# Performance work log

Hardware: AMD Instinct MI355X
Metric: run time of the kernel (lower is better)

## Reference

```python
import jax, jax.numpy as jnp
import numpy as np

B, S, D, H = 2, 2048, 1024, 16
HD = D // H

def setup_inputs() -> dict:
    key = jax.random.key(0)
    ks = jax.random.split(key, 5)
    sc = 1.0 / np.sqrt(D)
    return {
        "x": jax.random.normal(ks[0], (B, S, D), dtype=jnp.float32),
        "Wq": jax.random.normal(ks[1], (D, D), dtype=jnp.float32) * sc,
        "bq": jnp.zeros((D,), jnp.float32),
        "Wk": jax.random.normal(ks[2], (D, D), dtype=jnp.float32) * sc,
        "bk": jnp.zeros((D,), jnp.float32),
        "Wv": jax.random.normal(ks[3], (D, D), dtype=jnp.float32) * sc,
        "bv": jnp.zeros((D,), jnp.float32),
        "Wo": jax.random.normal(ks[4], (D, D), dtype=jnp.float32) * sc,
        "bo": jnp.zeros((D,), jnp.float32),
    }

def reference(x, Wq, bq, Wk, bk, Wv, bv, Wo, bo):
    b, s, d = x.shape
    def proj(W, bias):
        # [B,S,D] -> [B,H,S,HD]
        return (x @ W + bias).reshape(b, s, H, HD).swapaxes(1, 2)
    q = proj(Wq, bq)
    k = proj(Wk, bk)
    v = proj(Wv, bv)
    # naive full attention, matching the module (materializes [B,H,S,S])
    logits = jnp.einsum("bhqd,bhkd->bhqk", q, k) / jnp.sqrt(jnp.float32(HD))
    attn = jax.nn.softmax(logits, axis=-1)
    vals = jnp.einsum("bhqk,bhkd->bhqd", attn, v)
    vals = vals.swapaxes(1, 2).reshape(b, s, d)
    return vals @ Wo + bo
```

## Files before the change

### kernel.cpp

```cpp
#include <hip/hip_runtime.h>

typedef unsigned short u16;
typedef __bf16 bf16x8 __attribute__((ext_vector_type(8)));
typedef float f32x4 __attribute__((ext_vector_type(4)));

__device__ __forceinline__ u16 f2bf(float f) {
    union { float f; unsigned int i; } v;
    v.f = f;
    unsigned int u = v.i;
    return (u16)((u + 0x7fffu + ((u >> 16) & 1u)) >> 16);
}

__device__ __forceinline__ void dma16(const void* g, void* l) {
    __builtin_amdgcn_global_load_lds(
        (__attribute__((address_space(1))) void*)g,
        (__attribute__((address_space(3))) void*)l, 16, 0, 0);
}


__global__ __launch_bounds__(256) void cvt_w(const float* __restrict__ in,
                                             u16* __restrict__ out) {
    __shared__ u16 t[32][33];
    int bx = blockIdx.x * 32, by = blockIdx.y * 32;
    int tx = threadIdx.x & 31, ty = threadIdx.x >> 5;
#pragma unroll
    for (int i = 0; i < 32; i += 8)
        t[ty + i][tx] = f2bf(in[(size_t)(by + ty + i) * 1024 + bx + tx]);
    __syncthreads();
#pragma unroll
    for (int i = 0; i < 32; i += 8) {
        int n = bx + ty + i, k = by + tx;
        out[(size_t)n * 1024 + (k ^ ((n & 7) << 3))] = t[tx][ty + i];
    }
}

__global__ __launch_bounds__(256) void cvt_x(const float* __restrict__ in,
                                             u16* __restrict__ out) {
    int i = blockIdx.x * 256 + threadIdx.x;
    int s = i >> 8, k = (i & 255) * 4;
    float4 f = reinterpret_cast<const float4*>(in)[i];
    ushort4 h;
    h.x = f2bf(f.x); h.y = f2bf(f.y); h.z = f2bf(f.z); h.w = f2bf(f.w);
    *reinterpret_cast<ushort4*>(&out[(size_t)s * 1024 + (k ^ ((s & 7) << 3))]) = h;
}

__global__ __launch_bounds__(256) void gemm_qkv(
    const u16* __restrict__ xbf, const u16* __restrict__ wt,
    const float* __restrict__ bq, const float* __restrict__ bk,
    const float* __restrict__ bv,
    u16* __restrict__ qkg, u16* __restrict__ vgt) {
    __shared__ __align__(16) u16 As[128 * 64];
    __shared__ __align__(16) u16 Bs[128 * 64];

    int tid = threadIdx.x;
    int m0 = blockIdx.y * 128, n0 = blockIdx.x * 128;
    int wave = tid >> 6, lane = tid & 63;
    int wm = (wave >> 1) * 64, wn = (wave & 1) * 64;
    int l16 = lane & 15, quad = lane >> 4;
    int sl = l16 & 7;

    int seg = n0 >> 10;
    int n0r = n0 & 1023;
    const u16* WT = wt + (size_t)seg * 1048576;
    bool swp = (seg == 2);

    f32x4 acc[4][4];
#pragma unroll
    for (int mi = 0; mi < 4; mi++)
#pragma unroll
        for (int ni = 0; ni < 4; ni++) acc[mi][ni] = (f32x4){0.f, 0.f, 0.f, 0.f};

    int rsub = lane >> 3, c16 = (lane & 7) * 8;
    for (int k0 = 0; k0 < 1024; k0 += 64) {
#pragma unroll
        for (int i = 0; i < 4; i++) {
            int row = wave * 32 + i * 8 + rsub;
            dma16(&xbf[(size_t)(m0 + row) * 1024 + k0 + c16], &As[wave * 2048 + i * 512]);
            dma16(&WT[(size_t)(n0r + row) * 1024 + k0 + c16], &Bs[wave * 2048 + i * 512]);
        }
        __syncthreads();
        const u16* Am = swp ? Bs : As;
        const u16* Bn = swp ? As : Bs;
#pragma unroll
        for (int kk = 0; kk < 64; kk += 32) {
            int co = ((((kk >> 3) + quad) ^ sl) << 3);
            bf16x8 af[4], bf[4];
#pragma unroll
            for (int mi = 0; mi < 4; mi++)
                af[mi] = *reinterpret_cast<const bf16x8*>(
                    &Am[(wm + mi * 16 + l16) * 64 + co]);
#pragma unroll
            for (int ni = 0; ni < 4; ni++)
                bf[ni] = *reinterpret_cast<const bf16x8*>(
                    &Bn[(wn + ni * 16 + l16) * 64 + co]);
#pragma unroll
            for (int mi = 0; mi < 4; mi++)
#pragma unroll
                for (int ni = 0; ni < 4; ni++)
                    acc[mi][ni] = __builtin_amdgcn_mfma_f32_16x16x32_bf16(
                        af[mi], bf[ni], acc[mi][ni], 0, 0, 0);
        }
        __syncthreads();
    }

    if (!swp) {
#pragma unroll
        for (int ni = 0; ni < 4; ni++) {
            int n = n0 + wn + ni * 16 + l16;
            float bb = (n < 1024) ? bq[n] : bk[n - 1024];
#pragma unroll
            for (int mi = 0; mi < 4; mi++)
#pragma unroll
                for (int r = 0; r < 4; r++) {
                    int s = m0 + wm + mi * 16 + quad * 4 + r;
                    int col = n ^ ((s & 7) << 3);
                    qkg[(size_t)(s >> 11) * 4194304 + (size_t)(s & 2047) * 2048 + col] =
                        f2bf(acc[mi][ni][r] + bb);
                }
        }
    } else {
#pragma unroll
        for (int mi = 0; mi < 4; mi++)
#pragma unroll
            for (int r = 0; r < 4; r++) {
                int v = n0r + wm + mi * 16 + quad * 4 + r;
                float bb = bv[v];
#pragma unroll
                for (int ni = 0; ni < 4; ni++) {
                    int s = m0 + wn + ni * 16 + l16;
                    int scol = (s & 2047) ^ ((v & 7) << 3);
                    vgt[(size_t)((s >> 11) * 1024 + v) * 2048 + scol] =
                        f2bf(acc[mi][ni][r] + bb);
                }
            }
    }
}

#define SC2 0.18033688f

__global__ __launch_bounds__(256) void attention_kern(
    const u16* __restrict__ qkg, const u16* __restrict__ vgt,
    u16* __restrict__ att) {
    __shared__ __align__(16) u16 Qs[128 * 64];
    __shared__ __align__(16) u16 Ks[64 * 64];
    __shared__ __align__(16) u16 Vt[64 * 64];
    __shared__ __align__(16) u16 Ps[128 * 64];

    int tid = threadIdx.x;
    int qt = blockIdx.x, h = blockIdx.y, b = blockIdx.z;
    int wave = tid >> 6, lane = tid & 63;
    int l16 = lane & 15, quad = lane >> 4;
    int rsub = lane >> 3, c16 = (lane & 7) * 8;
    int sl = l16 & 7;
    int pl = (l16 >> 1) & 7;

    const u16* qb = qkg + (size_t)b * 4194304 + (size_t)(qt * 128) * 2048 + h * 64;
    const u16* kb = qkg + (size_t)b * 4194304 + 1024 + h * 64;
    const u16* vb = vgt + (size_t)(b * 1024 + h * 64) * 2048;

#pragma unroll
    for (int i = 0; i < 4; i++) {
        int row = wave * 32 + i * 8 + rsub;
        dma16(&qb[(size_t)row * 2048 + c16], &Qs[wave * 2048 + i * 512]);
    }

    float lp[2][4];
    f32x4 o[2][4];
#pragma unroll
    for (int mi = 0; mi < 2; mi++)
#pragma unroll
        for (int r = 0; r < 4; r++) lp[mi][r] = 0.f;
#pragma unroll
    for (int mi = 0; mi < 2; mi++)
#pragma unroll
        for (int ni = 0; ni < 4; ni++) o[mi][ni] = (f32x4){0.f, 0.f, 0.f, 0.f};

    for (int kt = 0; kt < 32; kt++) {
        const u16* ktb = kb + (size_t)(kt * 64) * 2048;
        const u16* vtb = vb + kt * 64;
#pragma unroll
        for (int i = 0; i < 2; i++) {
            int row = wave * 16 + i * 8 + rsub;
            dma16(&ktb[(size_t)row * 2048 + c16], &Ks[wave * 1024 + i * 512]);
            dma16(&vtb[(size_t)row * 2048 + c16], &Vt[wave * 1024 + i * 512]);
        }
        __syncthreads();

        f32x4 s[2][4];
#pragma unroll
        for (int mi = 0; mi < 2; mi++)
#pragma unroll
            for (int ni = 0; ni < 4; ni++) s[mi][ni] = (f32x4){0.f, 0.f, 0.f, 0.f};
#pragma unroll
        for (int kk = 0; kk < 64; kk += 32) {
            int co = ((((kk >> 3) + quad) ^ sl) << 3);
            bf16x8 af[2], bf[4];
#pragma unroll
            for (int mi = 0; mi < 2; mi++)
                af[mi] = *reinterpret_cast<const bf16x8*>(
                    &Qs[(wave * 32 + mi * 16 + l16) * 64 + co]);
#pragma unroll
            for (int ni = 0; ni < 4; ni++)
                bf[ni] = *reinterpret_cast<const bf16x8*>(
                    &Ks[(ni * 16 + l16) * 64 + co]);
#pragma unroll
            for (int mi = 0; mi < 2; mi++)
#pragma unroll
                for (int ni = 0; ni < 4; ni++)
                    s[mi][ni] = __builtin_amdgcn_mfma_f32_16x16x32_bf16(
                        af[mi], bf[ni], s[mi][ni], 0, 0, 0);
        }

#pragma unroll
        for (int mi = 0; mi < 2; mi++)
#pragma unroll
            for (int r = 0; r < 4; r++) {
                int row = wave * 32 + mi * 16 + quad * 4 + r;
                int wkey = (quad * 2 + (r >> 1)) & 7;
                float rs = 0.f;
#pragma unroll
                for (int ni = 0; ni < 4; ni++) {
                    float p = exp2f(s[mi][ni][r] * SC2);
                    rs += p;
                    int cch = 2 * ni + (l16 >> 3);
                    Ps[row * 64 + ((cch ^ wkey) << 3) + (l16 & 7)] = f2bf(p);
                }
                lp[mi][r] += rs;
            }

#pragma unroll
        for (int kk = 0; kk < 64; kk += 32) {
            int ch = (kk >> 3) + quad;
            int coP = ((ch ^ pl) << 3);
            int coV = ((ch ^ sl) << 3);
            bf16x8 af[2], bf[4];
#pragma unroll
            for (int mi = 0; mi < 2; mi++)
                af[mi] = *reinterpret_cast<const bf16x8*>(
                    &Ps[(wave * 32 + mi * 16 + l16) * 64 + coP]);
#pragma unroll
            for (int ni = 0; ni < 4; ni++)
                bf[ni] = *reinterpret_cast<const bf16x8*>(
                    &Vt[(ni * 16 + l16) * 64 + coV]);
#pragma unroll
            for (int mi = 0; mi < 2; mi++)
#pragma unroll
                for (int ni = 0; ni < 4; ni++)
                    o[mi][ni] = __builtin_amdgcn_mfma_f32_16x16x32_bf16(
                        af[mi], bf[ni], o[mi][ni], 0, 0, 0);
        }
        __syncthreads();
    }

    float lr[2][4];
#pragma unroll
    for (int mi = 0; mi < 2; mi++)
#pragma unroll
        for (int r = 0; r < 4; r++) {
            float v = lp[mi][r];
#pragma unroll
            for (int off = 1; off < 16; off <<= 1) v += __shfl_xor(v, off);
            lr[mi][r] = v;
        }
#pragma unroll
    for (int mi = 0; mi < 2; mi++)
#pragma unroll
        for (int ni = 0; ni < 4; ni++)
#pragma unroll
            for (int r = 0; r < 4; r++) {
                int srow = b * 2048 + qt * 128 + wave * 32 + mi * 16 + quad * 4 + r;
                int d = h * 64 + ni * 16 + l16;
                att[(size_t)srow * 1024 + (d ^ ((srow & 7) << 3))] =
                    f2bf(o[mi][ni][r] / lr[mi][r]);
            }
}

__global__ __launch_bounds__(256) void gemm_out(
    const u16* __restrict__ attb, const u16* __restrict__ wot,
    const float* __restrict__ bo, float* __restrict__ out) {
    __shared__ __align__(16) u16 As[128 * 64];
    __shared__ __align__(16) u16 Bs[128 * 64];

    int tid = threadIdx.x;
    int m0 = blockIdx.y * 128, n0 = blockIdx.x * 128;
    int wave = tid >> 6, lane = tid & 63;
    int wm = (wave >> 1) * 64, wn = (wave & 1) * 64;
    int l16 = lane & 15, quad = lane >> 4;
    int sl = l16 & 7;
    int rsub = lane >> 3, c16 = (lane & 7) * 8;

    f32x4 acc[4][4];
#pragma unroll
    for (int mi = 0; mi < 4; mi++)
#pragma unroll
        for (int ni = 0; ni < 4; ni++) acc[mi][ni] = (f32x4){0.f, 0.f, 0.f, 0.f};

    for (int k0 = 0; k0 < 1024; k0 += 64) {
#pragma unroll
        for (int i = 0; i < 4; i++) {
            int row = wave * 32 + i * 8 + rsub;
            dma16(&attb[(size_t)(m0 + row) * 1024 + k0 + c16], &As[wave * 2048 + i * 512]);
            dma16(&wot[(size_t)(n0 + row) * 1024 + k0 + c16], &Bs[wave * 2048 + i * 512]);
        }
        __syncthreads();
#pragma unroll
        for (int kk = 0; kk < 64; kk += 32) {
            int co = ((((kk >> 3) + quad) ^ sl) << 3);
            bf16x8 af[4], bf[4];
#pragma unroll
            for (int mi = 0; mi < 4; mi++)
                af[mi] = *reinterpret_cast<const bf16x8*>(
                    &As[(wm + mi * 16 + l16) * 64 + co]);
#pragma unroll
            for (int ni = 0; ni < 4; ni++)
                bf[ni] = *reinterpret_cast<const bf16x8*>(
                    &Bs[(wn + ni * 16 + l16) * 64 + co]);
#pragma unroll
            for (int mi = 0; mi < 4; mi++)
#pragma unroll
                for (int ni = 0; ni < 4; ni++)
                    acc[mi][ni] = __builtin_amdgcn_mfma_f32_16x16x32_bf16(
                        af[mi], bf[ni], acc[mi][ni], 0, 0, 0);
        }
        __syncthreads();
    }

#pragma unroll
    for (int ni = 0; ni < 4; ni++) {
        int n = n0 + wn + ni * 16 + l16;
        float bb = bo[n];
#pragma unroll
        for (int mi = 0; mi < 4; mi++)
#pragma unroll
            for (int r = 0; r < 4; r++)
                out[(size_t)(m0 + wm + mi * 16 + quad * 4 + r) * 1024 + n] =
                    acc[mi][ni][r] + bb;
    }
}

extern "C" void kernel_launch(void* const* d_in, const int* in_sizes, int n_in,
                              void* d_out, int out_size, void* d_ws, size_t ws_size,
                              hipStream_t stream) {
    const float* x  = (const float*)d_in[0];
    const float* Wq = (const float*)d_in[1];
    const float* bq = (const float*)d_in[2];
    const float* Wk = (const float*)d_in[3];
    const float* bk = (const float*)d_in[4];
    const float* Wv = (const float*)d_in[5];
    const float* bv = (const float*)d_in[6];
    const float* Wo = (const float*)d_in[7];
    const float* bo = (const float*)d_in[8];

    u16* WT  = (u16*)d_out;
    u16* xbf = (u16*)d_out + 4 * 1048576;
    u16* ATT = xbf;
    u16* QKg = (u16*)d_ws;
    u16* Vgt = (u16*)d_ws + 8 * 1048576;

    dim3 tg(32, 32);
    cvt_w<<<tg, 256, 0, stream>>>(Wq, WT);
    cvt_w<<<tg, 256, 0, stream>>>(Wk, WT + 1048576);
    cvt_w<<<tg, 256, 0, stream>>>(Wv, WT + 2 * 1048576);
    cvt_x<<<4096, 256, 0, stream>>>(x, xbf);

    gemm_qkv<<<dim3(24, 32), 256, 0, stream>>>(xbf, WT, bq, bk, bv, QKg, Vgt);

    attention_kern<<<dim3(16, 16, 2), 256, 0, stream>>>(QKg, Vgt, ATT);

    hipMemcpyAsync(QKg, ATT, (size_t)8 * 1048576, hipMemcpyDeviceToDevice, stream);
    cvt_w<<<tg, 256, 0, stream>>>(Wo, (u16*)d_ws + 4 * 1048576);
    gemm_out<<<dim3(8, 32), 256, 0, stream>>>(
        (u16*)d_ws, (u16*)d_ws + 4 * 1048576, bo, (float*)d_out);
}
```

Before: 243.3 us.

## Halve attention query tile, batch weight conversions, shrink output GEMM tile

The attention kernel now processes 64 query rows per block instead of 128, doubling the grid so more blocks can be resident. It also uses hardware exp2 and rcp, packs the P stores into vectorised bf16x4 writes, and re-swizzles K rows to avoid LDS bank conflicts. The four weight conversions are fused into one launch, and Wo is converted early and then copied into the workspace. The output GEMM uses 128x64 tiles for more blocks. The cost is that K and V tiles are reloaded twice as often per query, and there is an extra device copy.

```diff
diff --git a/kernel.cpp b/kernel.cpp
--- a/kernel.cpp
+++ b/kernel.cpp
@@ -2,6 +2,7 @@
 
 typedef unsigned short u16;
 typedef __bf16 bf16x8 __attribute__((ext_vector_type(8)));
+typedef __bf16 bf16x4 __attribute__((ext_vector_type(4)));
 typedef float f32x4 __attribute__((ext_vector_type(4)));
 
 __device__ __forceinline__ u16 f2bf(float f) {
@@ -18,9 +19,14 @@
 }
 
 
-__global__ __launch_bounds__(256) void cvt_w(const float* __restrict__ in,
-                                             u16* __restrict__ out) {
+__global__ __launch_bounds__(256) void cvt_w4(
+    const float* __restrict__ W0, const float* __restrict__ W1,
+    const float* __restrict__ W2, const float* __restrict__ W3,
+    u16* __restrict__ out) {
     __shared__ u16 t[32][33];
+    int z = blockIdx.z;
+    const float* in = (z == 0) ? W0 : (z == 1) ? W1 : (z == 2) ? W2 : W3;
+    u16* o = out + (size_t)z * 1048576;
     int bx = blockIdx.x * 32, by = blockIdx.y * 32;
     int tx = threadIdx.x & 31, ty = threadIdx.x >> 5;
 #pragma unroll
@@ -30,7 +36,7 @@
 #pragma unroll
     for (int i = 0; i < 32; i += 8) {
         int n = bx + ty + i, k = by + tx;
-        out[(size_t)n * 1024 + (k ^ ((n & 7) << 3))] = t[tx][ty + i];
+        o[(size_t)n * 1024 + (k ^ ((n & 7) << 3))] = t[tx][ty + i];
     }
 }
 
@@ -141,10 +147,10 @@
 __global__ __launch_bounds__(256) void attention_kern(
     const u16* __restrict__ qkg, const u16* __restrict__ vgt,
     u16* __restrict__ att) {
-    __shared__ __align__(16) u16 Qs[128 * 64];
+    __shared__ __align__(16) u16 Qs[64 * 64];
     __shared__ __align__(16) u16 Ks[64 * 64];
     __shared__ __align__(16) u16 Vt[64 * 64];
-    __shared__ __align__(16) u16 Ps[128 * 64];
+    __shared__ __align__(16) u16 Ps[64 * 64];
 
     int tid = threadIdx.x;
     int qt = blockIdx.x, h = blockIdx.y, b = blockIdx.z;
@@ -152,173 +158,149 @@
     int l16 = lane & 15, quad = lane >> 4;
     int rsub = lane >> 3, c16 = (lane & 7) * 8;
     int sl = l16 & 7;
-    int pl = (l16 >> 1) & 7;
-
-    const u16* qb = qkg + (size_t)b * 4194304 + (size_t)(qt * 128) * 2048 + h * 64;
+
+    const u16* qb = qkg + (size_t)b * 4194304 + (size_t)(qt * 64) * 2048 + h * 64;
     const u16* kb = qkg + (size_t)b * 4194304 + 1024 + h * 64;
     const u16* vb = vgt + (size_t)(b * 1024 + h * 64) * 2048;
 
 #pragma unroll
-    for (int i = 0; i < 4; i++) {
-        int row = wave * 32 + i * 8 + rsub;
-        dma16(&qb[(size_t)row * 2048 + c16], &Qs[wave * 2048 + i * 512]);
-    }
-
-    float lp[2][4];
-    f32x4 o[2][4];
-#pragma unroll
-    for (int mi = 0; mi < 2; mi++)
-#pragma unroll
-        for (int r = 0; r < 4; r++) lp[mi][r] = 0.f;
-#pragma unroll
-    for (int mi = 0; mi < 2; mi++)
-#pragma unroll
-        for (int ni = 0; ni < 4; ni++) o[mi][ni] = (f32x4){0.f, 0.f, 0.f, 0.f};
+    for (int i = 0; i < 2; i++) {
+        int row = wave * 16 + i * 8 + rsub;
+        dma16(&qb[(size_t)row * 2048 + c16], &Qs[wave * 1024 + i * 512]);
+    }
+
+    float lp[4];
+    f32x4 o[4];
+#pragma unroll
+    for (int r = 0; r < 4; r++) lp[r] = 0.f;
+#pragma unroll
+    for (int ni = 0; ni < 4; ni++) o[ni] = (f32x4){0.f, 0.f, 0.f, 0.f};
 
     for (int kt = 0; kt < 32; kt++) {
         const u16* ktb = kb + (size_t)(kt * 64) * 2048;
         const u16* vtb = vb + kt * 64;
 #pragma unroll
         for (int i = 0; i < 2; i++) {
-            int row = wave * 16 + i * 8 + rsub;
-            dma16(&ktb[(size_t)row * 2048 + c16], &Ks[wave * 1024 + i * 512]);
-            dma16(&vtb[(size_t)row * 2048 + c16], &Vt[wave * 1024 + i * 512]);
-        }
-        __syncthreads();
-
-        f32x4 s[2][4];
-#pragma unroll
-        for (int mi = 0; mi < 2; mi++)
-#pragma unroll
-            for (int ni = 0; ni < 4; ni++) s[mi][ni] = (f32x4){0.f, 0.f, 0.f, 0.f};
+            int gk = 32 * i + 4 * rsub + wave;
+            dma16(&ktb[(size_t)gk * 2048 + c16], &Ks[wave * 1024 + i * 512]);
+            int rv = wave * 16 + i * 8 + rsub;
+            dma16(&vtb[(size_t)rv * 2048 + c16], &Vt[wave * 1024 + i * 512]);
+        }
+        __syncthreads();
+
+        f32x4 s[4];
+#pragma unroll
+        for (int ni = 0; ni < 4; ni++) s[ni] = (f32x4){0.f, 0.f, 0.f, 0.f};
+#pragma unroll
+        for (int kk = 0; kk < 64; kk += 32) {
+            int lg = (kk >> 3) + quad;
+            bf16x8 af = *reinterpret_cast<const bf16x8*>(
+                &Qs[(wave * 16 + l16) * 64 + ((lg ^ sl) << 3)]);
+#pragma unroll
+            for (int ni = 0; ni < 4; ni++) {
+                int bkey = 4 * (l16 & 1) + ni;
+                bf16x8 bf = *reinterpret_cast<const bf16x8*>(
+                    &Ks[(ni * 16 + l16) * 64 + ((lg ^ bkey) << 3)]);
+                s[ni] = __builtin_amdgcn_mfma_f32_16x16x32_bf16(af, bf, s[ni], 0, 0, 0);
+            }
+        }
+
+#pragma unroll
+        for (int r = 0; r < 4; r++) {
+            float p0 = __builtin_amdgcn_exp2f(s[0][r] * SC2);
+            float p1 = __builtin_amdgcn_exp2f(s[1][r] * SC2);
+            float p2 = __builtin_amdgcn_exp2f(s[2][r] * SC2);
+            float p3 = __builtin_amdgcn_exp2f(s[3][r] * SC2);
+            lp[r] += (p0 + p1) + (p2 + p3);
+            f32x4 pf = {p0, p1, p2, p3};
+            bf16x4 pb = __builtin_convertvector(pf, bf16x4);
+            int q = wave * 16 + quad * 4 + r;
+            *reinterpret_cast<bf16x4*>(
+                &Ps[q * 64 + (((l16 >> 1) ^ (q & 7)) << 3) + (l16 & 1) * 4]) = pb;
+        }
+
 #pragma unroll
         for (int kk = 0; kk < 64; kk += 32) {
             int co = ((((kk >> 3) + quad) ^ sl) << 3);
-            bf16x8 af[2], bf[4];
-#pragma unroll
-            for (int mi = 0; mi < 2; mi++)
-                af[mi] = *reinterpret_cast<const bf16x8*>(
-                    &Qs[(wave * 32 + mi * 16 + l16) * 64 + co]);
-#pragma unroll
-            for (int ni = 0; ni < 4; ni++)
-                bf[ni] = *reinterpret_cast<const bf16x8*>(
-                    &Ks[(ni * 16 + l16) * 64 + co]);
-#pragma unroll
-            for (int mi = 0; mi < 2; mi++)
-#pragma unroll
-                for (int ni = 0; ni < 4; ni++)
-                    s[mi][ni] = __builtin_amdgcn_mfma_f32_16x16x32_bf16(
-                        af[mi], bf[ni], s[mi][ni], 0, 0, 0);
-        }
-
-#pragma unroll
-        for (int mi = 0; mi < 2; mi++)
-#pragma unroll
-            for (int r = 0; r < 4; r++) {
-                int row = wave * 32 + mi * 16 + quad * 4 + r;
-                int wkey = (quad * 2 + (r >> 1)) & 7;
-                float rs = 0.f;
-#pragma unroll
-                for (int ni = 0; ni < 4; ni++) {
-                    float p = exp2f(s[mi][ni][r] * SC2);
-                    rs += p;
-                    int cch = 2 * ni + (l16 >> 3);
-                    Ps[row * 64 + ((cch ^ wkey) << 3) + (l16 & 7)] = f2bf(p);
-                }
-                lp[mi][r] += rs;
+            bf16x8 af = *reinterpret_cast<const bf16x8*>(
+                &Ps[(wave * 16 + l16) * 64 + co]);
+#pragma unroll
+            for (int ni = 0; ni < 4; ni++) {
+                bf16x8 bf = *reinterpret_cast<const bf16x8*>(
+                    &Vt[(ni * 16 + l16) * 64 + co]);
+                o[ni] = __builtin_amdgcn_mfma_f32_16x16x32_bf16(af, bf, o[ni], 0, 0, 0);
             }
-
-#pragma unroll
-        for (int kk = 0; kk < 64; kk += 32) {
-            int ch = (kk >> 3) + quad;
-            int coP = ((ch ^ pl) << 3);
-            int coV = ((ch ^ sl) << 3);
-            bf16x8 af[2], bf[4];
-#pragma unroll
-            for (int mi = 0; mi < 2; mi++)
-                af[mi] = *reinterpret_cast<const bf16x8*>(
-                    &Ps[(wave * 32 + mi * 16 + l16) * 64 + coP]);
-#pragma unroll
-            for (int ni = 0; ni < 4; ni++)
-                bf[ni] = *reinterpret_cast<const bf16x8*>(
-                    &Vt[(ni * 16 + l16) * 64 + coV]);
-#pragma unroll
-            for (int mi = 0; mi < 2; mi++)
-#pragma unroll
-                for (int ni = 0; ni < 4; ni++)
-                    o[mi][ni] = __builtin_amdgcn_mfma_f32_16x16x32_bf16(
-                        af[mi], bf[ni], o[mi][ni], 0, 0, 0);
-        }
-        __syncthreads();
-    }
-
-    float lr[2][4];
-#pragma unroll
-    for (int mi = 0; mi < 2; mi++)
+        }
+        __syncthreads();
+    }
+
+    float inv[4];
+#pragma unroll
+    for (int r = 0; r < 4; r++) {
+        float v = lp[r];
+#pragma unroll
+        for (int off = 1; off < 16; off <<= 1) v += __shfl_xor(v, off);
+        inv[r] = __builtin_amdgcn_rcpf(v);
+    }
+#pragma unroll
+    for (int ni = 0; ni < 4; ni++)
 #pragma unroll
         for (int r = 0; r < 4; r++) {
-            float v = lp[mi][r];
-#pragma unroll
-            for (int off = 1; off < 16; off <<= 1) v += __shfl_xor(v, off);
-            lr[mi][r] = v;
-        }
-#pragma unroll
-    for (int mi = 0; mi < 2; mi++)
-#pragma unroll
-        for (int ni = 0; ni < 4; ni++)
-#pragma unroll
-            for (int r = 0; r < 4; r++) {
-                int srow = b * 2048 + qt * 128 + wave * 32 + mi * 16 + quad * 4 + r;
-                int d = h * 64 + ni * 16 + l16;
-                att[(size_t)srow * 1024 + (d ^ ((srow & 7) << 3))] =
-                    f2bf(o[mi][ni][r] / lr[mi][r]);
-            }
+            int srow = b * 2048 + qt * 64 + wave * 16 + quad * 4 + r;
+            int d = h * 64 + ni * 16 + l16;
+            att[(size_t)srow * 1024 + (d ^ ((srow & 7) << 3))] =
+                f2bf(o[ni][r] * inv[r]);
+        }
 }
 
 __global__ __launch_bounds__(256) void gemm_out(
     const u16* __restrict__ attb, const u16* __restrict__ wot,
     const float* __restrict__ bo, float* __restrict__ out) {
     __shared__ __align__(16) u16 As[128 * 64];
-    __shared__ __align__(16) u16 Bs[128 * 64];
+    __shared__ __align__(16) u16 Bs[64 * 64];
 
     int tid = threadIdx.x;
-    int m0 = blockIdx.y * 128, n0 = blockIdx.x * 128;
+    int m0 = blockIdx.y * 128, n0 = blockIdx.x * 64;
     int wave = tid >> 6, lane = tid & 63;
-    int wm = (wave >> 1) * 64, wn = (wave & 1) * 64;
+    int wm = (wave >> 1) * 64, wn = (wave & 1) * 32;
     int l16 = lane & 15, quad = lane >> 4;
     int sl = l16 & 7;
     int rsub = lane >> 3, c16 = (lane & 7) * 8;
 
-    f32x4 acc[4][4];
+    f32x4 acc[4][2];
 #pragma unroll
     for (int mi = 0; mi < 4; mi++)
 #pragma unroll
-        for (int ni = 0; ni < 4; ni++) acc[mi][ni] = (f32x4){0.f, 0.f, 0.f, 0.f};
+        for (int ni = 0; ni < 2; ni++) acc[mi][ni] = (f32x4){0.f, 0.f, 0.f, 0.f};
 
     for (int k0 = 0; k0 < 1024; k0 += 64) {
 #pragma unroll
         for (int i = 0; i < 4; i++) {
             int row = wave * 32 + i * 8 + rsub;
             dma16(&attb[(size_t)(m0 + row) * 1024 + k0 + c16], &As[wave * 2048 + i * 512]);
-            dma16(&wot[(size_t)(n0 + row) * 1024 + k0 + c16], &Bs[wave * 2048 + i * 512]);
+        }
+#pragma unroll
+        for (int i = 0; i < 2; i++) {
+            int row = wave * 16 + i * 8 + rsub;
+            dma16(&wot[(size_t)(n0 + row) * 1024 + k0 + c16], &Bs[wave * 1024 + i * 512]);
         }
         __syncthreads();
 #pragma unroll
         for (int kk = 0; kk < 64; kk += 32) {
             int co = ((((kk >> 3) + quad) ^ sl) << 3);
-            bf16x8 af[4], bf[4];
+            bf16x8 af[4], bf[2];
 #pragma unroll
             for (int mi = 0; mi < 4; mi++)
                 af[mi] = *reinterpret_cast<const bf16x8*>(
                     &As[(wm + mi * 16 + l16) * 64 + co]);
 #pragma unroll
-            for (int ni = 0; ni < 4; ni++)
+            for (int ni = 0; ni < 2; ni++)
                 bf[ni] = *reinterpret_cast<const bf16x8*>(
                     &Bs[(wn + ni * 16 + l16) * 64 + co]);
 #pragma unroll
             for (int mi = 0; mi < 4; mi++)
 #pragma unroll
-                for (int ni = 0; ni < 4; ni++)
+                for (int ni = 0; ni < 2; ni++)
                     acc[mi][ni] = __builtin_amdgcn_mfma_f32_16x16x32_bf16(
                         af[mi], bf[ni], acc[mi][ni], 0, 0, 0);
         }
@@ -326,7 +308,7 @@
     }
 
 #pragma unroll
-    for (int ni = 0; ni < 4; ni++) {
+    for (int ni = 0; ni < 2; ni++) {
         int n = n0 + wn + ni * 16 + l16;
         float bb = bo[n];
 #pragma unroll
@@ -357,18 +339,16 @@
     u16* QKg = (u16*)d_ws;
     u16* Vgt = (u16*)d_ws + 8 * 1048576;
 
-    dim3 tg(32, 32);
-    cvt_w<<<tg, 256, 0, stream>>>(Wq, WT);
-    cvt_w<<<tg, 256, 0, stream>>>(Wk, WT + 1048576);
-    cvt_w<<<tg, 256, 0, stream>>>(Wv, WT + 2 * 1048576);
+    cvt_w4<<<dim3(32, 32, 4), 256, 0, stream>>>(Wq, Wk, Wv, Wo, WT);
     cvt_x<<<4096, 256, 0, stream>>>(x, xbf);
 
     gemm_qkv<<<dim3(24, 32), 256, 0, stream>>>(xbf, WT, bq, bk, bv, QKg, Vgt);
 
-    attention_kern<<<dim3(16, 16, 2), 256, 0, stream>>>(QKg, Vgt, ATT);
+    attention_kern<<<dim3(32, 16, 2), 256, 0, stream>>>(QKg, Vgt, ATT);
 
     hipMemcpyAsync(QKg, ATT, (size_t)8 * 1048576, hipMemcpyDeviceToDevice, stream);
-    cvt_w<<<tg, 256, 0, stream>>>(Wo, (u16*)d_ws + 4 * 1048576);
-    gemm_out<<<dim3(8, 32), 256, 0, stream>>>(
-        (u16*)d_ws, (u16*)d_ws + 4 * 1048576, bo, (float*)d_out);
-}
+    hipMemcpyAsync(Vgt, WT + 3 * 1048576, (size_t)2 * 1048576,
+                   hipMemcpyDeviceToDevice, stream);
+    gemm_out<<<dim3(16, 32), 256, 0, stream>>>(
+        (u16*)d_ws, Vgt, bo, (float*)d_out);
+}
```

After: 219.1 us. 1.11x faster.
